# Kernel tuning notes

Hardware: AMD Instinct MI355X
Metric: run time of the kernel (lower is better)

## Reference

```python
import jax, jax.numpy as jnp
import numpy as np

# Fixed problem sizes (uniform frames so the irregular loop vectorizes)
S = 32            # number of frames (sequences)
N = 128           # pedestrians per frame
H = 64            # pool_h_dim (lstm hidden dim)
G = 8             # grid_size
NS = 2.0          # neighbourhood_size
OUT = 64          # pool_out_dim
EPS = 1e-5        # BatchNorm1d eps


def setup_inputs() -> dict:
    key = jax.random.key(0)
    k1, k2, k3 = jax.random.split(key, 3)
    hidden_states = jax.random.normal(k1, (S * N, H), jnp.float32)
    # positions in [0, 4): neighbourhood of size 2 captures many neighbours
    all_pos = jax.random.uniform(k2, (S * N, 2), jnp.float32) * 4.0
    W = jax.random.normal(k3, (G * G * H, OUT), jnp.float32) * 0.02
    b = jnp.zeros((OUT,), jnp.float32)
    gamma = jnp.ones((OUT,), jnp.float32)
    beta = jnp.zeros((OUT,), jnp.float32)
    starts = jnp.arange(S, dtype=jnp.int32) * N
    seq_start_end = jnp.stack([starts, starts + N], axis=1)
    return {"hidden_states": hidden_states, "all_pos": all_pos, "W": W,
            "b": b, "gamma": gamma, "beta": beta,
            "seq_start_end": seq_start_end}


def _pool_one_frame(hs, ps):
    # hs: [N, H] hidden states, ps: [N, 2] positions of one frame.
    # Pair (i, j): bbox around ped i, contribution from ped j's hidden state.
    xi, yi = ps[:, 0][:, None], ps[:, 1][:, None]   # bbox owner i -> rows
    xj, yj = ps[:, 0][None, :], ps[:, 1][None, :]   # neighbour j -> cols
    half = NS / 2
    tlx, tly = xi - half, yi + half                 # top-left of bbox(i)
    brx, bry = xi + half, yi - half                 # bottom-right of bbox(i)
    gx = jnp.floor((xj - tlx) / NS * G)
    gy = jnp.floor((tly - yj) / NS * G)
    grid = (gx + G * gy).astype(jnp.int32) + 1      # +1: slot 0 is dump bin
    # out-of-bbox or self -> masked to bin 0
    mask = ((xj <= tlx) | (yj >= tly) | (xj >= brx) | (yj <= bry)
            | jnp.eye(N, dtype=bool))
    grid = grid + (jnp.arange(N, dtype=jnp.int32) * (G * G))[:, None]
    grid = jnp.where(mask, 0, grid)                 # [N, N]
    vals = jnp.broadcast_to(hs[None, :, :], (N, N, H)).reshape(N * N, H)
    pooled = jax.ops.segment_sum(vals, grid.reshape(-1),
                                 num_segments=N * G * G + 1)[1:]
    return pooled.reshape(N, G * G * H)


def reference(hidden_states, all_pos, W, b, gamma, beta, seq_start_end):
    h = hidden_states.reshape(S, N, H)
    p = all_pos.reshape(S, N, 2)
    pool_h = jax.vmap(_pool_one_frame)(h, p).reshape(S * N, G * G * H)
    x = pool_h @ W + b
    # BatchNorm1d in training mode: biased batch statistics
    mean = jnp.mean(x, axis=0)
    var = jnp.mean((x - mean) ** 2, axis=0)
    x = (x - mean) / jnp.sqrt(var + EPS) * gamma + beta
    return jax.nn.relu(x)
```

## Files before the change

### kernel.cpp

```cpp
#include <hip/hip_runtime.h>
#include <math.h>

#define NFRAMES 32
#define NPED    128
#define HDIM    64
#define KDIM    4096
#define OUTD    64
#define EPSV    1e-5f
#define NBLK    256
#define PROW    4104
#define HROW    136

typedef __attribute__((ext_vector_type(8))) short  short8;
typedef __attribute__((ext_vector_type(4))) float  floatx4;

static __device__ __forceinline__ unsigned short f2bf(float f) {
    union { float f; unsigned u; } v; v.f = f;
    unsigned r = v.u + 0x7fffu + ((v.u >> 16) & 1u);
    return (unsigned short)(r >> 16);
}

static __device__ __forceinline__ int kperm(int k) {
    return (k & 0xC0F) | ((k >> 2) & 0x0F0) | ((k & 0x030) << 4);
}

__global__ void k_wt(const float* __restrict__ W, unsigned short* __restrict__ Wt) {
    __shared__ float T[64 * 65];
    const int t  = threadIdx.x;
    const int k0 = blockIdx.x * 64;
    #pragma unroll
    for (int it = 0; it < 16; ++it) {
        int idx = it * 256 + t;
        int kl = idx >> 6, o = idx & 63;
        T[kl * 65 + o] = W[(size_t)(k0 + kl) * OUTD + o];
    }
    __syncthreads();
    #pragma unroll
    for (int it = 0; it < 8; ++it) {
        int idx = it * 256 + t;
        int o = idx >> 5, kl = (idx & 31) * 2;
        unsigned v = (unsigned)f2bf(T[kl * 65 + o]) |
                     ((unsigned)f2bf(T[(kl + 1) * 65 + o]) << 16);
        *(unsigned*)(Wt + (size_t)o * KDIM + kperm(k0 + kl)) = v;
    }
}

__global__ __launch_bounds__(256, 1) void k_fused(
    const float* __restrict__ hs, const float* __restrict__ pos,
    const unsigned short* __restrict__ Wt,
    float* __restrict__ x, float* __restrict__ psumT, float* __restrict__ psumsqT)
{
    __shared__ unsigned short P[16 * PROW];
    __shared__ unsigned short HsT[HDIM * HROW];
    __shared__ unsigned char  CT[16 * NPED];
    __shared__ float posL[NPED * 2];

    const int tid   = threadIdx.x;
    const int bid   = blockIdx.x;
    const int f     = bid >> 3;
    const int chunk = bid & 7;
    const int lane  = tid & 63;
    const int w     = tid >> 6;
    const int m     = lane & 15;
    const int quad  = lane >> 4;

    posL[tid] = pos[f * (NPED * 2) + tid];
    const float* hsF = hs + f * (NPED * HDIM);
    #pragma unroll
    for (int it = 0; it < 8; ++it) {
        int g = it * 256 + tid;
        float4 v = ((const float4*)hsF)[g];
        int j  = g >> 4;
        int h0 = (g & 15) * 4;
        HsT[(h0 + 0) * HROW + j] = f2bf(v.x);
        HsT[(h0 + 1) * HROW + j] = f2bf(v.y);
        HsT[(h0 + 2) * HROW + j] = f2bf(v.z);
        HsT[(h0 + 3) * HROW + j] = f2bf(v.w);
    }
    __syncthreads();

    const int i0 = chunk * 16;
    #pragma unroll
    for (int it = 0; it < 8; ++it) {
        int idx = it * 256 + tid;
        int i = idx >> 7, j = idx & 127;
        float xi = posL[(i0 + i) * 2], yi = posL[(i0 + i) * 2 + 1];
        float xj = posL[j * 2],        yj = posL[j * 2 + 1];
        float tlx = xi - 1.0f, tly = yi + 1.0f;
        bool valid = (xj > tlx) & (yj < tly) & (xj < xi + 1.0f) &
                     (yj > yi - 1.0f) & (j != i0 + i);
        int gx = (int)floorf((xj - tlx) * 4.0f);
        int gy = (int)floorf((tly - yj) * 4.0f);
        int c  = gx + 8 * gy;
        CT[i * NPED + j] = (valid && (unsigned)c < 64u) ? (unsigned char)c : 255;
    }

    short8 Af[4][4];
    #pragma unroll
    for (int ht = 0; ht < 4; ++ht)
        #pragma unroll
        for (int kt = 0; kt < 4; ++kt)
            Af[ht][kt] = *(const short8*)&HsT[(ht * 16 + m) * HROW + kt * 32 + quad * 8];
    __syncthreads();

    #pragma unroll
    for (int r = 0; r < 4; ++r) {
        const int i = w * 4 + r;
        const unsigned char* ctRow = CT + i * NPED;
        #pragma unroll
        for (int ct = 0; ct < 4; ++ct) {
            const unsigned tgt = (unsigned)(ct * 16 + m);
            floatx4 pa[4];
            #pragma unroll
            for (int ht = 0; ht < 4; ++ht) pa[ht] = (floatx4){0.f, 0.f, 0.f, 0.f};
            #pragma unroll
            for (int kt = 0; kt < 4; ++kt) {
                unsigned long long cb = *(const unsigned long long*)(ctRow + kt * 32 + quad * 8);
                unsigned lo32 = (unsigned)cb, hi32 = (unsigned)(cb >> 32);
                union { int iv[4]; short8 sv; } B;
                B.iv[0] = (((lo32      ) & 0xFFu) == tgt ? 0x00003F80 : 0) |
                          (((lo32 >>  8) & 0xFFu) == tgt ? 0x3F800000 : 0);
                B.iv[1] = (((lo32 >> 16) & 0xFFu) == tgt ? 0x00003F80 : 0) |
                          (((lo32 >> 24)        ) == tgt ? 0x3F800000 : 0);
                B.iv[2] = (((hi32      ) & 0xFFu) == tgt ? 0x00003F80 : 0) |
                          (((hi32 >>  8) & 0xFFu) == tgt ? 0x3F800000 : 0);
                B.iv[3] = (((hi32 >> 16) & 0xFFu) == tgt ? 0x00003F80 : 0) |
                          (((hi32 >> 24)        ) == tgt ? 0x3F800000 : 0);
                #pragma unroll
                for (int ht = 0; ht < 4; ++ht)
                    pa[ht] = __builtin_amdgcn_mfma_f32_16x16x32_bf16(Af[ht][kt], B.sv, pa[ht], 0, 0, 0);
            }
            #pragma unroll
            for (int ht = 0; ht < 4; ++ht) {
                union { floatx4 fv; unsigned uv[4]; } U; U.fv = pa[ht];
                uint2 pv;
                pv.x = __builtin_amdgcn_perm(U.uv[1], U.uv[0], 0x07060302u);
                pv.y = __builtin_amdgcn_perm(U.uv[3], U.uv[2], 0x07060302u);
                *reinterpret_cast<uint2*>(&P[i * PROW + ct * 1024 + ht * 256 + m * 16 + quad * 4]) = pv;
            }
        }
    }
    __syncthreads();

    floatx4 acc[4];
    #pragma unroll
    for (int u = 0; u < 4; ++u) acc[u] = (floatx4){0.f, 0.f, 0.f, 0.f};
    const unsigned short* Prow  = P + m * PROW;
    const unsigned short* WtRow = Wt + (size_t)(w * 16 + m) * KDIM;
    #pragma unroll 4
    for (int kk = 0; kk < KDIM; kk += 128) {
        #pragma unroll
        for (int u = 0; u < 4; ++u) {
            int k0 = kk + u * 32 + quad * 8;
            short8 a = *(const short8*)(Prow + k0);
            short8 b = *(const short8*)(WtRow + k0);
            acc[u] = __builtin_amdgcn_mfma_f32_16x16x32_bf16(a, b, acc[u], 0, 0, 0);
        }
    }

    floatx4 accf = (acc[0] + acc[1]) + (acc[2] + acc[3]);
    const int ibase = f * NPED + chunk * 16;
    float s1 = 0.f, s2 = 0.f;
    #pragma unroll
    for (int r = 0; r < 4; ++r) {
        float v = accf[r];
        int row = quad * 4 + r;
        x[(size_t)(ibase + row) * OUTD + w * 16 + m] = v;
        s1 += v; s2 += v * v;
    }
    s1 += __shfl_xor(s1, 16); s1 += __shfl_xor(s1, 32);
    s2 += __shfl_xor(s2, 16); s2 += __shfl_xor(s2, 32);
    if (lane < 16) {
        psumT  [(w * 16 + lane) * NBLK + bid] = s1;
        psumsqT[(w * 16 + lane) * NBLK + bid] = s2;
    }
}

__global__ void k_stats(const float* __restrict__ psumT, const float* __restrict__ psumsqT,
                        float* __restrict__ mean, float* __restrict__ invstd) {
    int o = blockIdx.x;
    int t = threadIdx.x;
    float s1 = 0.f, s2 = 0.f;
    #pragma unroll
    for (int i = 0; i < NBLK / 64; ++i) {
        s1 += psumT [o * NBLK + i * 64 + t];
        s2 += psumsqT[o * NBLK + i * 64 + t];
    }
    #pragma unroll
    for (int d = 1; d < 64; d <<= 1) {
        s1 += __shfl_xor(s1, d);
        s2 += __shfl_xor(s2, d);
    }
    if (t == 0) {
        const float inv_n = 1.0f / (float)(NFRAMES * NPED);
        float mu  = s1 * inv_n;
        float var = s2 * inv_n - mu * mu;
        mean[o]   = mu;
        invstd[o] = rsqrtf(var + EPSV);
    }
}

__global__ void k_apply(const float* __restrict__ x, const float* __restrict__ mean,
                        const float* __restrict__ invstd, const float* __restrict__ gamma,
                        const float* __restrict__ beta, float* __restrict__ out) {
    int g = blockIdx.x * 256 + threadIdx.x;
    int oq = g & 15;
    float4 xv = ((const float4*)x)[g];
    float4 mu = ((const float4*)mean)[oq];
    float4 is = ((const float4*)invstd)[oq];
    float4 ga = ((const float4*)gamma)[oq];
    float4 be = ((const float4*)beta)[oq];
    float4 r;
    r.x = (xv.x - mu.x) * is.x * ga.x + be.x;
    r.y = (xv.y - mu.y) * is.y * ga.y + be.y;
    r.z = (xv.z - mu.z) * is.z * ga.z + be.z;
    r.w = (xv.w - mu.w) * is.w * ga.w + be.w;
    r.x = r.x > 0.f ? r.x : 0.f;
    r.y = r.y > 0.f ? r.y : 0.f;
    r.z = r.z > 0.f ? r.z : 0.f;
    r.w = r.w > 0.f ? r.w : 0.f;
    ((float4*)out)[g] = r;
}

extern "C" void kernel_launch(void* const* d_in, const int* in_sizes, int n_in,
                              void* d_out, int out_size, void* d_ws, size_t ws_size,
                              hipStream_t stream) {
    const float* hs    = (const float*)d_in[0];
    const float* pos   = (const float*)d_in[1];
    const float* W     = (const float*)d_in[2];
    const float* gamma = (const float*)d_in[4];
    const float* beta  = (const float*)d_in[5];

    char* ws = (char*)d_ws;
    unsigned short* Wt = (unsigned short*)ws;
    float* x       = (float*)(ws + (512 << 10));
    float* psumT   = (float*)(ws + (512 << 10) + (1 << 20));
    float* psumsqT = psumT + NBLK * OUTD;
    float* mean    = psumsqT + NBLK * OUTD;
    float* invstd  = mean + OUTD;

    k_wt   <<<KDIM / 64, 256, 0, stream>>>(W, Wt);
    k_fused<<<NBLK, 256, 0, stream>>>(hs, pos, Wt, x, psumT, psumsqT);
    k_stats<<<OUTD, 64, 0, stream>>>(psumT, psumsqT, mean, invstd);
    k_apply<<<(NFRAMES * NPED * OUTD / 4) / 256, 256, 0, stream>>>(x, mean, invstd, gamma, beta,
                                                                   (float*)d_out);
}
```

Before: 94.25 us.

## Double fused-kernel threads with split-K, fold stats into last block, vectorize Wt stores

The fused kernel now runs 512 threads per block. The pooling stage reorders its loops so each CT byte row is decoded once for all four column tiles. The GEMM is split across two wave halves along K, and the halves are combined through shared memory. The separate stats kernel is removed: an atomic counter elects the last finishing block to reduce the per-block partial sums into mean and invstd. The weight transpose kernel now writes 16-byte vector stores and resets the counter. This adds waves for latency hiding and removes one launch, at the cost of an extra shared-memory reduction, a fence and atomic, and a serial tail in the last block.

```diff
diff --git a/kernel.cpp b/kernel.cpp
--- a/kernel.cpp
+++ b/kernel.cpp
@@ -24,10 +24,12 @@
     return (k & 0xC0F) | ((k >> 2) & 0x0F0) | ((k & 0x030) << 4);
 }
 
-__global__ void k_wt(const float* __restrict__ W, unsigned short* __restrict__ Wt) {
+__global__ void k_wt(const float* __restrict__ W, unsigned short* __restrict__ Wt,
+                     unsigned int* __restrict__ counter) {
     __shared__ float T[64 * 65];
     const int t  = threadIdx.x;
     const int k0 = blockIdx.x * 64;
+    if (blockIdx.x == 0 && t == 0) *counter = 0u;
     #pragma unroll
     for (int it = 0; it < 16; ++it) {
         int idx = it * 256 + t;
@@ -35,25 +37,34 @@
         T[kl * 65 + o] = W[(size_t)(k0 + kl) * OUTD + o];
     }
     __syncthreads();
-    #pragma unroll
-    for (int it = 0; it < 8; ++it) {
-        int idx = it * 256 + t;
-        int o = idx >> 5, kl = (idx & 31) * 2;
-        unsigned v = (unsigned)f2bf(T[kl * 65 + o]) |
-                     ((unsigned)f2bf(T[(kl + 1) * 65 + o]) << 16);
-        *(unsigned*)(Wt + (size_t)o * KDIM + kperm(k0 + kl)) = v;
-    }
-}
-
-__global__ __launch_bounds__(256, 1) void k_fused(
+    {
+        int o   = t & 63;
+        int seg = t >> 6;
+        int kl  = seg * 16;
+        unsigned pk[8];
+        #pragma unroll
+        for (int e = 0; e < 8; ++e) {
+            pk[e] = (unsigned)f2bf(T[(kl + 2 * e) * 65 + o]) |
+                    ((unsigned)f2bf(T[(kl + 2 * e + 1) * 65 + o]) << 16);
+        }
+        unsigned short* dst = Wt + (size_t)o * KDIM + kperm(k0 + kl);
+        ((uint4*)dst)[0] = (uint4){pk[0], pk[1], pk[2], pk[3]};
+        ((uint4*)dst)[1] = (uint4){pk[4], pk[5], pk[6], pk[7]};
+    }
+}
+
+__global__ __launch_bounds__(512, 2) void k_fused(
     const float* __restrict__ hs, const float* __restrict__ pos,
     const unsigned short* __restrict__ Wt,
-    float* __restrict__ x, float* __restrict__ psumT, float* __restrict__ psumsqT)
+    float* __restrict__ x, float* __restrict__ psumT, float* __restrict__ psumsqT,
+    float* __restrict__ mean, float* __restrict__ invstd,
+    unsigned int* __restrict__ counter)
 {
     __shared__ unsigned short P[16 * PROW];
     __shared__ unsigned short HsT[HDIM * HROW];
     __shared__ unsigned char  CT[16 * NPED];
     __shared__ float posL[NPED * 2];
+    __shared__ int isLast;
 
     const int tid   = threadIdx.x;
     const int bid   = blockIdx.x;
@@ -64,11 +75,11 @@
     const int m     = lane & 15;
     const int quad  = lane >> 4;
 
-    posL[tid] = pos[f * (NPED * 2) + tid];
+    if (tid < 256) posL[tid] = pos[f * (NPED * 2) + tid];
     const float* hsF = hs + f * (NPED * HDIM);
     #pragma unroll
-    for (int it = 0; it < 8; ++it) {
-        int g = it * 256 + tid;
+    for (int it = 0; it < 4; ++it) {
+        int g = it * 512 + tid;
         float4 v = ((const float4*)hsF)[g];
         int j  = g >> 4;
         int h0 = (g & 15) * 4;
@@ -81,8 +92,8 @@
 
     const int i0 = chunk * 16;
     #pragma unroll
-    for (int it = 0; it < 8; ++it) {
-        int idx = it * 256 + tid;
+    for (int it = 0; it < 4; ++it) {
+        int idx = it * 512 + tid;
         int i = idx >> 7, j = idx & 127;
         float xi = posL[(i0 + i) * 2], yi = posL[(i0 + i) * 2 + 1];
         float xj = posL[j * 2],        yj = posL[j * 2 + 1];
@@ -104,51 +115,57 @@
     __syncthreads();
 
     #pragma unroll
-    for (int r = 0; r < 4; ++r) {
-        const int i = w * 4 + r;
+    for (int r = 0; r < 2; ++r) {
+        const int i = w * 2 + r;
         const unsigned char* ctRow = CT + i * NPED;
-        #pragma unroll
-        for (int ct = 0; ct < 4; ++ct) {
-            const unsigned tgt = (unsigned)(ct * 16 + m);
-            floatx4 pa[4];
-            #pragma unroll
-            for (int ht = 0; ht < 4; ++ht) pa[ht] = (floatx4){0.f, 0.f, 0.f, 0.f};
-            #pragma unroll
-            for (int kt = 0; kt < 4; ++kt) {
-                unsigned long long cb = *(const unsigned long long*)(ctRow + kt * 32 + quad * 8);
-                unsigned lo32 = (unsigned)cb, hi32 = (unsigned)(cb >> 32);
+        floatx4 pa[4][4];
+        #pragma unroll
+        for (int ht = 0; ht < 4; ++ht)
+            #pragma unroll
+            for (int ct = 0; ct < 4; ++ct) pa[ht][ct] = (floatx4){0.f, 0.f, 0.f, 0.f};
+        #pragma unroll
+        for (int kt = 0; kt < 4; ++kt) {
+            unsigned long long cb = *(const unsigned long long*)(ctRow + kt * 32 + quad * 8);
+            unsigned lo = (unsigned)cb, hi = (unsigned)(cb >> 32);
+            int b0 = (int)(lo & 255u), b1 = (int)((lo >> 8) & 255u);
+            int b2 = (int)((lo >> 16) & 255u), b3 = (int)(lo >> 24);
+            int b4 = (int)(hi & 255u), b5 = (int)((hi >> 8) & 255u);
+            int b6 = (int)((hi >> 16) & 255u), b7 = (int)(hi >> 24);
+            #pragma unroll
+            for (int ct = 0; ct < 4; ++ct) {
+                const int tgt = ct * 16 + m;
                 union { int iv[4]; short8 sv; } B;
-                B.iv[0] = (((lo32      ) & 0xFFu) == tgt ? 0x00003F80 : 0) |
-                          (((lo32 >>  8) & 0xFFu) == tgt ? 0x3F800000 : 0);
-                B.iv[1] = (((lo32 >> 16) & 0xFFu) == tgt ? 0x00003F80 : 0) |
-                          (((lo32 >> 24)        ) == tgt ? 0x3F800000 : 0);
-                B.iv[2] = (((hi32      ) & 0xFFu) == tgt ? 0x00003F80 : 0) |
-                          (((hi32 >>  8) & 0xFFu) == tgt ? 0x3F800000 : 0);
-                B.iv[3] = (((hi32 >> 16) & 0xFFu) == tgt ? 0x00003F80 : 0) |
-                          (((hi32 >> 24)        ) == tgt ? 0x3F800000 : 0);
+                B.iv[0] = (b0 == tgt ? 0x00003F80 : 0) | (b1 == tgt ? 0x3F800000 : 0);
+                B.iv[1] = (b2 == tgt ? 0x00003F80 : 0) | (b3 == tgt ? 0x3F800000 : 0);
+                B.iv[2] = (b4 == tgt ? 0x00003F80 : 0) | (b5 == tgt ? 0x3F800000 : 0);
+                B.iv[3] = (b6 == tgt ? 0x00003F80 : 0) | (b7 == tgt ? 0x3F800000 : 0);
                 #pragma unroll
                 for (int ht = 0; ht < 4; ++ht)
-                    pa[ht] = __builtin_amdgcn_mfma_f32_16x16x32_bf16(Af[ht][kt], B.sv, pa[ht], 0, 0, 0);
-            }
+                    pa[ht][ct] = __builtin_amdgcn_mfma_f32_16x16x32_bf16(Af[ht][kt], B.sv, pa[ht][ct], 0, 0, 0);
+            }
+        }
+        #pragma unroll
+        for (int ct = 0; ct < 4; ++ct)
             #pragma unroll
             for (int ht = 0; ht < 4; ++ht) {
-                union { floatx4 fv; unsigned uv[4]; } U; U.fv = pa[ht];
+                union { floatx4 fv; unsigned uv[4]; } U; U.fv = pa[ht][ct];
                 uint2 pv;
                 pv.x = __builtin_amdgcn_perm(U.uv[1], U.uv[0], 0x07060302u);
                 pv.y = __builtin_amdgcn_perm(U.uv[3], U.uv[2], 0x07060302u);
                 *reinterpret_cast<uint2*>(&P[i * PROW + ct * 1024 + ht * 256 + m * 16 + quad * 4]) = pv;
             }
-        }
-    }
-    __syncthreads();
-
+    }
+    __syncthreads();
+
+    const int wn = w & 3;
+    const int wh = w >> 2;
     floatx4 acc[4];
     #pragma unroll
     for (int u = 0; u < 4; ++u) acc[u] = (floatx4){0.f, 0.f, 0.f, 0.f};
-    const unsigned short* Prow  = P + m * PROW;
-    const unsigned short* WtRow = Wt + (size_t)(w * 16 + m) * KDIM;
+    const unsigned short* Prow  = P + m * PROW + wh * 2048;
+    const unsigned short* WtRow = Wt + (size_t)(wn * 16 + m) * KDIM + wh * 2048;
     #pragma unroll 4
-    for (int kk = 0; kk < KDIM; kk += 128) {
+    for (int kk = 0; kk < 2048; kk += 128) {
         #pragma unroll
         for (int u = 0; u < 4; ++u) {
             int k0 = kk + u * 32 + quad * 8;
@@ -157,46 +174,59 @@
             acc[u] = __builtin_amdgcn_mfma_f32_16x16x32_bf16(a, b, acc[u], 0, 0, 0);
         }
     }
-
     floatx4 accf = (acc[0] + acc[1]) + (acc[2] + acc[3]);
-    const int ibase = f * NPED + chunk * 16;
-    float s1 = 0.f, s2 = 0.f;
-    #pragma unroll
-    for (int r = 0; r < 4; ++r) {
-        float v = accf[r];
-        int row = quad * 4 + r;
-        x[(size_t)(ibase + row) * OUTD + w * 16 + m] = v;
-        s1 += v; s2 += v * v;
-    }
-    s1 += __shfl_xor(s1, 16); s1 += __shfl_xor(s1, 32);
-    s2 += __shfl_xor(s2, 16); s2 += __shfl_xor(s2, 32);
-    if (lane < 16) {
-        psumT  [(w * 16 + lane) * NBLK + bid] = s1;
-        psumsqT[(w * 16 + lane) * NBLK + bid] = s2;
-    }
-}
-
-__global__ void k_stats(const float* __restrict__ psumT, const float* __restrict__ psumsqT,
-                        float* __restrict__ mean, float* __restrict__ invstd) {
-    int o = blockIdx.x;
-    int t = threadIdx.x;
-    float s1 = 0.f, s2 = 0.f;
-    #pragma unroll
-    for (int i = 0; i < NBLK / 64; ++i) {
-        s1 += psumT [o * NBLK + i * 64 + t];
-        s2 += psumsqT[o * NBLK + i * 64 + t];
-    }
-    #pragma unroll
-    for (int d = 1; d < 64; d <<= 1) {
-        s1 += __shfl_xor(s1, d);
-        s2 += __shfl_xor(s2, d);
-    }
-    if (t == 0) {
-        const float inv_n = 1.0f / (float)(NFRAMES * NPED);
-        float mu  = s1 * inv_n;
-        float var = s2 * inv_n - mu * mu;
-        mean[o]   = mu;
-        invstd[o] = rsqrtf(var + EPSV);
+
+    float* red = (float*)HsT;
+    if (wh == 1) *(floatx4*)(red + (wn * 64 + lane) * 4) = accf;
+    __syncthreads();
+
+    if (wh == 0) {
+        accf += *(const floatx4*)(red + (wn * 64 + lane) * 4);
+        const int ibase = f * NPED + chunk * 16;
+        float s1 = 0.f, s2 = 0.f;
+        #pragma unroll
+        for (int r = 0; r < 4; ++r) {
+            float v = accf[r];
+            int row = quad * 4 + r;
+            x[(size_t)(ibase + row) * OUTD + wn * 16 + m] = v;
+            s1 += v; s2 += v * v;
+        }
+        s1 += __shfl_xor(s1, 16); s1 += __shfl_xor(s1, 32);
+        s2 += __shfl_xor(s2, 16); s2 += __shfl_xor(s2, 32);
+        if (lane < 16) {
+            psumT  [(wn * 16 + lane) * NBLK + bid] = s1;
+            psumsqT[(wn * 16 + lane) * NBLK + bid] = s2;
+        }
+    }
+
+    __threadfence();
+    __syncthreads();
+    if (tid == 0) isLast = (atomicAdd(counter, 1u) == (unsigned)(NBLK - 1)) ? 1 : 0;
+    __syncthreads();
+    if (isLast) {
+        __threadfence();
+        #pragma unroll
+        for (int oo = 0; oo < 8; ++oo) {
+            int o = w * 8 + oo;
+            float s1 = 0.f, s2 = 0.f;
+            #pragma unroll
+            for (int i2 = 0; i2 < 4; ++i2) {
+                s1 += psumT  [o * NBLK + i2 * 64 + lane];
+                s2 += psumsqT[o * NBLK + i2 * 64 + lane];
+            }
+            #pragma unroll
+            for (int d = 1; d < 64; d <<= 1) {
+                s1 += __shfl_xor(s1, d);
+                s2 += __shfl_xor(s2, d);
+            }
+            if (lane == 0) {
+                const float inv_n = 1.0f / (float)(NFRAMES * NPED);
+                float mu  = s1 * inv_n;
+                float var = s2 * inv_n - mu * mu;
+                mean[o]   = mu;
+                invstd[o] = rsqrtf(var + EPSV);
+            }
+        }
     }
 }
 
@@ -238,10 +268,10 @@
     float* psumsqT = psumT + NBLK * OUTD;
     float* mean    = psumsqT + NBLK * OUTD;
     float* invstd  = mean + OUTD;
-
-    k_wt   <<<KDIM / 64, 256, 0, stream>>>(W, Wt);
-    k_fused<<<NBLK, 256, 0, stream>>>(hs, pos, Wt, x, psumT, psumsqT);
-    k_stats<<<OUTD, 64, 0, stream>>>(psumT, psumsqT, mean, invstd);
+    unsigned int* counter = (unsigned int*)(invstd + OUTD);
+
+    k_wt   <<<KDIM / 64, 256, 0, stream>>>(W, Wt, counter);
+    k_fused<<<NBLK, 512, 0, stream>>>(hs, pos, Wt, x, psumT, psumsqT, mean, invstd, counter);
     k_apply<<<(NFRAMES * NPED * OUTD / 4) / 256, 256, 0, stream>>>(x, mean, invstd, gamma, beta,
                                                                    (float*)d_out);
 }
```

Result: slower. 139.0 us (+47.5%).
